# Kernel tuning notes

Hardware: AMD Instinct MI355X
Metric: run time of the kernel (lower is better)

Reference implementation:

```python
import jax, jax.numpy as jnp
import numpy as np

# Module hyperparameters (from init_kwargs)
C = 128        # in_channel
L = 16         # seq_len
K = 7          # filter_size
DIL = 1        # dilation
G = 4          # num_groups
SPAN = (K - 1) * DIL + 1
PAD = (SPAN - 1) // 2

B, H, W = 8, 56, 56


def setup_inputs() -> dict:
    key = jax.random.key(0)
    k1, k2 = jax.random.split(key)
    x = jax.random.normal(k1, (B, C, L, H, W), dtype=jnp.float32)
    # kaiming_normal(mode='fan_out', nonlinearity='relu'):
    # fan_out = shape[0] * K * K, std = sqrt(2 / fan_out)
    std = (2.0 / (C * K * K)) ** 0.5
    filter_weight = jax.random.normal(k2, (C, L, K, K), dtype=jnp.float32) * std
    return {"x": x, "filter_weight": filter_weight}


def reference(x, filter_weight):
    # x: (B, C, T, H, W) ; filter_weight: (C, T, K, K)
    b, c, t, h, w = x.shape
    # zero-pad spatial dims
    x2 = jnp.pad(x, ((0, 0), (0, 0), (0, 0), (PAD, PAD), (PAD, PAD)))
    # x1: temporally shifted input (frame t-1, first frame duplicated)
    x1 = jnp.concatenate([x[:, :, :1], x[:, :, :-1]], axis=2)

    outs = []
    # static K*K offset loop (dy slow, dx fast -> matches torch meshgrid 'ij' flatten order)
    for dy in range(0, SPAN, DIL):
        for dx in range(0, SPAN, DIL):
            w_ct = filter_weight[:, :, dy // DIL, dx // DIL]  # (C, T)
            shifted = jax.lax.slice(
                x2, (0, 0, 0, dy, dx), (b, c, t, dy + h, dx + w))
            prod = w_ct[None, :, :, None, None] * x1 * shifted  # (B,C,T,H,W)
            # groupwise channel mean -> (B, G, T, H, W)
            resp = prod.reshape(b, G, c // G, t, h, w).mean(axis=2)
            outs.append(resp)
    # concat over offsets along channel dim -> (B, K^2*G, T, H, W)
    return jnp.concatenate(outs, axis=1)
```

## Files before the change

kernel.cpp:

```cpp
#include <hip/hip_runtime.h>
#include <cstdint>

#define C_ 128
#define L_ 16
#define G_ 4
#define H_ 56
#define W_ 56
#define HW_ 3136
#define CH_ 4
#define NCK_ 8
#define RS_ 64
#define XS_F (CH_ * 14 * RS_)
#define LDS_F (2 * XS_F)
#define PAD_F 6656

typedef float f4 __attribute__((ext_vector_type(4)));
typedef __attribute__((address_space(3))) uint32_t lds_u32;
typedef const __attribute__((address_space(1))) uint32_t glb_u32;

__global__ __launch_bounds__(448, 2)
void wcorr(const float* __restrict__ x, const float* __restrict__ wgt,
           float* __restrict__ out) {
  __shared__ float lds[LDS_F];
  __shared__ float lds_pad[PAD_F];
  asm volatile("" :: "v"(&lds_pad[threadIdx.x & 63]));

  int bid = blockIdx.x;
  int wid = (bid & 7) * 448 + (bid >> 3);
  int htile = wid % 7;
  int rest = wid / 7;
  int t = rest & 15;
  int bg = rest >> 4;
  int g = bg & 3;
  int b = bg >> 2;
  int h0 = htile * 8;

  int tid = threadIdx.x;
  int lane = tid & 63;
  int dyu = __builtin_amdgcn_readfirstlane(tid >> 6);
  int tx = lane & 7;
  int h = lane >> 3;
  bool wr = (tx < 7);
  int txc = wr ? tx : 6;
  int w0 = 8 * txc;
  int r = h + dyu;
  int t1 = (t > 0) ? (t - 1) : 0;

  for (int i = tid; i < LDS_F; i += 448) lds[i] = 0.0f;

  const size_t cstride = (size_t)L_ * HW_;
  const float* xg = x + ((size_t)b * C_ + (size_t)g * 32) * cstride;
  const float* x1b = xg + (size_t)t1 * HW_ + (size_t)(h0 + h) * W_ + w0;
  const float* wgb = wgt + (size_t)(g * 32) * (L_ * 49) + t * 49 + dyu * 7;

  auto stage = [&](int tau, int k) {
    int fb = (k & 1) * XS_F;
    int c0 = k * CH_;
    int rho = tau >> 4;
    int sb = tau & 15;
    int ci = rho / 14;
    int rr = rho - ci * 14;
    int vb = sb ^ (rr & 7);
    int hh = h0 - 3 + rr;
    bool ok = (vb >= 1) && (vb <= 14) && (hh >= 0) && (hh < H_);
    const float* src = xg + (size_t)(c0 + ci) * cstride + (size_t)t * HW_
                          + hh * W_ + (vb * 4 - 4);
    float* dst = &lds[fb + (tau & ~63) * 4];
    if (ok)
      __builtin_amdgcn_global_load_lds((glb_u32*)src, (lds_u32*)dst, 16, 0, 0);
  };

  float acc[7][8];
  #pragma unroll
  for (int i = 0; i < 7; ++i)
    #pragma unroll
    for (int p = 0; p < 8; ++p) acc[i][p] = 0.0f;

  __syncthreads();
  stage(tid, 0);
  stage(tid + 448, 0);
  __syncthreads();

  #pragma unroll 2
  for (int k = 0; k < NCK_; ++k) {
    if (k + 1 < NCK_) {
      stage(tid, k + 1);
      stage(tid + 448, k + 1);
    }
    int fb = (k & 1) * XS_F;
    int c0 = k * CH_;
    int s = r & 7;
    #pragma unroll
    for (int ci = 0; ci < CH_; ++ci) {
      const f4* xsrow = (const f4*)&lds[fb + (ci * 14 + r) * RS_];
      f4 q0 = xsrow[(2 * txc + 0) ^ s];
      f4 q1 = xsrow[(2 * txc + 1) ^ s];
      f4 q2 = xsrow[(2 * txc + 2) ^ s];
      f4 q3 = xsrow[(2 * txc + 3) ^ s];
      const float* x1p = x1b + (size_t)(c0 + ci) * cstride;
      f4 a0 = *(const f4*)(x1p);
      f4 a1 = *(const f4*)(x1p + 4);
      const float* wp = wgb + (size_t)(c0 + ci) * (L_ * 49);
      float w7[7];
      #pragma unroll
      for (int d = 0; d < 7; ++d) w7[d] = wp[d];
      float rr_[16] = {q0.x, q0.y, q0.z, q0.w, q1.x, q1.y, q1.z, q1.w,
                       q2.x, q2.y, q2.z, q2.w, q3.x, q3.y, q3.z, q3.w};
      float x1v[8] = {a0.x, a0.y, a0.z, a0.w, a1.x, a1.y, a1.z, a1.w};
      #pragma unroll
      for (int dxx = 0; dxx < 7; ++dxx) {
        #pragma unroll
        for (int p = 0; p < 8; ++p) {
          acc[dxx][p] = fmaf(w7[dxx], x1v[p] * rr_[p + dxx + 1], acc[dxx][p]);
        }
      }
    }
    __syncthreads();
  }

  if (wr) {
    const float sc = 1.0f / 32.0f;
    #pragma unroll
    for (int dxx = 0; dxx < 7; ++dxx) {
      int och = (dyu * 7 + dxx) * G_ + g;
      float* op = out + (((size_t)b * 196 + och) * L_ + t) * (size_t)HW_
                      + (size_t)(h0 + h) * W_ + w0;
      f4 o0 = {acc[dxx][0] * sc, acc[dxx][1] * sc,
               acc[dxx][2] * sc, acc[dxx][3] * sc};
      f4 o1 = {acc[dxx][4] * sc, acc[dxx][5] * sc,
               acc[dxx][6] * sc, acc[dxx][7] * sc};
      __builtin_nontemporal_store(o0, (f4*)op);
      __builtin_nontemporal_store(o1, (f4*)(op + 4));
    }
  }
}

extern "C" void kernel_launch(void* const* d_in, const int* in_sizes, int n_in,
                              void* d_out, int out_size, void* d_ws, size_t ws_size,
                              hipStream_t stream) {
  const float* x = (const float*)d_in[0];
  const float* w = (const float*)d_in[1];
  float* o = (float*)d_out;
  dim3 grid(3584), block(448);
  hipLaunchKernelGGL(wcorr, grid, block, 0, stream, x, w, o);
}
```

Measured before the change: 244.6 us.

## Halve row tile, stage filter weights in LDS, and remap threads to 256-wide blocks

Each block now covers 4 output rows instead of 8 and uses 256 threads, with each wave holding several dy/h slots, so the grid doubles to 7168 blocks. The per-(c,dy) filter weights are prescaled by 1/32 and preloaded into LDS once per block, replacing per-thread global weight loads. The x tile is padded to a 68-float row stride in place of the XOR swizzle. Idle lanes rise (dy==7 slots and tx==7 lanes), the halo rows are reloaded more often relative to output, and the unswizzled layout may cause LDS bank conflicts.

```diff
diff --git a/kernel.cpp b/kernel.cpp
--- a/kernel.cpp
+++ b/kernel.cpp
@@ -9,16 +9,19 @@
 #define HW_ 3136
 #define CH_ 4
 #define NCK_ 8
-#define RS_ 64
-#define XS_F (CH_ * 14 * RS_)
-#define LDS_F (2 * XS_F)
-#define PAD_F 6656
+#define RS_ 68
+#define NROW_ 10
+#define XS_F (CH_ * NROW_ * RS_)
+#define XTASK_ (CH_ * NROW_ * 17)
+#define WL_F 2048
+#define LDS_F (WL_F + 2 * XS_F)
+#define PAD_F 768
 
 typedef float f4 __attribute__((ext_vector_type(4)));
 typedef __attribute__((address_space(3))) uint32_t lds_u32;
 typedef const __attribute__((address_space(1))) uint32_t glb_u32;
 
-__global__ __launch_bounds__(448, 2)
+__global__ __launch_bounds__(256, 2)
 void wcorr(const float* __restrict__ x, const float* __restrict__ wgt,
            float* __restrict__ out) {
   __shared__ float lds[LDS_F];
@@ -26,48 +29,69 @@
   asm volatile("" :: "v"(&lds_pad[threadIdx.x & 63]));
 
   int bid = blockIdx.x;
-  int wid = (bid & 7) * 448 + (bid >> 3);
-  int htile = wid % 7;
-  int rest = wid / 7;
+  int wid = (bid & 7) * 896 + (bid >> 3);
+  int htile = wid % 14;
+  int rest = wid / 14;
   int t = rest & 15;
   int bg = rest >> 4;
   int g = bg & 3;
   int b = bg >> 2;
-  int h0 = htile * 8;
+  int h0 = htile * 4;
 
   int tid = threadIdx.x;
-  int lane = tid & 63;
-  int dyu = __builtin_amdgcn_readfirstlane(tid >> 6);
-  int tx = lane & 7;
-  int h = lane >> 3;
-  bool wr = (tx < 7);
-  int txc = wr ? tx : 6;
+  int tx = tid & 7;
+  int slot = tid >> 3;
+  int h = slot & 3;
+  int dy = slot >> 2;
+  bool active = (dy < 7) && (tx < 7);
+  int dyc = dy < 7 ? dy : 6;
+  int txc = tx < 7 ? tx : 6;
+  int r = h + dyc;
+  int t1 = t > 0 ? t - 1 : 0;
   int w0 = 8 * txc;
-  int r = h + dyu;
-  int t1 = (t > 0) ? (t - 1) : 0;
 
-  for (int i = tid; i < LDS_F; i += 448) lds[i] = 0.0f;
+  for (int i = tid; i < LDS_F; i += 256) lds[i] = 0.0f;
+  __syncthreads();
 
   const size_t cstride = (size_t)L_ * HW_;
   const float* xg = x + ((size_t)b * C_ + (size_t)g * 32) * cstride;
   const float* x1b = xg + (size_t)t1 * HW_ + (size_t)(h0 + h) * W_ + w0;
-  const float* wgb = wgt + (size_t)(g * 32) * (L_ * 49) + t * 49 + dyu * 7;
 
-  auto stage = [&](int tau, int k) {
-    int fb = (k & 1) * XS_F;
+  {
+    const float sc = 1.0f / 32.0f;
+    const float* wsrc = wgt + (size_t)(g * 32) * (L_ * 49) + t * 49;
+    #pragma unroll
+    for (int j = 0; j < 8; ++j) {
+      int idx = tid + j * 256;
+      int c = idx >> 6;
+      int rem = idx & 63;
+      int dyy = rem >> 3, dxx = rem & 7;
+      float v = 0.0f;
+      if (dyy < 7 && dxx < 7)
+        v = wsrc[(size_t)c * (L_ * 49) + dyy * 7 + dxx] * sc;
+      lds[idx] = v;
+    }
+  }
+
+  auto stage = [&](int tau, int k, bool on) {
+    int fb = WL_F + (k & 1) * XS_F;
     int c0 = k * CH_;
-    int rho = tau >> 4;
-    int sb = tau & 15;
-    int ci = rho / 14;
-    int rr = rho - ci * 14;
-    int vb = sb ^ (rr & 7);
+    int row = (tau * 965) >> 14;
+    int vb = tau - row * 17;
+    int ci = (row * 205) >> 11;
+    int rr = row - ci * 10;
     int hh = h0 - 3 + rr;
-    bool ok = (vb >= 1) && (vb <= 14) && (hh >= 0) && (hh < H_);
+    bool ok = on && (vb >= 1) && (vb <= 14) && (hh >= 0) && (hh < H_);
     const float* src = xg + (size_t)(c0 + ci) * cstride + (size_t)t * HW_
                           + hh * W_ + (vb * 4 - 4);
     float* dst = &lds[fb + (tau & ~63) * 4];
     if (ok)
       __builtin_amdgcn_global_load_lds((glb_u32*)src, (lds_u32*)dst, 16, 0, 0);
+  };
+  auto stage_chunk = [&](int k) {
+    stage(tid, k, true);
+    stage(tid + 256, k, true);
+    stage(tid + 512, k, tid + 512 < XTASK_);
   };
 
   float acc[7][8];
@@ -76,34 +100,28 @@
     #pragma unroll
     for (int p = 0; p < 8; ++p) acc[i][p] = 0.0f;
 
-  __syncthreads();
-  stage(tid, 0);
-  stage(tid + 448, 0);
+  stage_chunk(0);
   __syncthreads();
 
   #pragma unroll 2
   for (int k = 0; k < NCK_; ++k) {
-    if (k + 1 < NCK_) {
-      stage(tid, k + 1);
-      stage(tid + 448, k + 1);
-    }
-    int fb = (k & 1) * XS_F;
+    if (k + 1 < NCK_) stage_chunk(k + 1);
+    int fb = WL_F + (k & 1) * XS_F;
     int c0 = k * CH_;
-    int s = r & 7;
     #pragma unroll
     for (int ci = 0; ci < CH_; ++ci) {
-      const f4* xsrow = (const f4*)&lds[fb + (ci * 14 + r) * RS_];
-      f4 q0 = xsrow[(2 * txc + 0) ^ s];
-      f4 q1 = xsrow[(2 * txc + 1) ^ s];
-      f4 q2 = xsrow[(2 * txc + 2) ^ s];
-      f4 q3 = xsrow[(2 * txc + 3) ^ s];
+      const f4* xsrow = (const f4*)&lds[fb + (ci * NROW_ + r) * RS_];
+      f4 q0 = xsrow[2 * txc + 0];
+      f4 q1 = xsrow[2 * txc + 1];
+      f4 q2 = xsrow[2 * txc + 2];
+      f4 q3 = xsrow[2 * txc + 3];
+      const f4* wl = (const f4*)&lds[(c0 + ci) * 64 + dyc * 8];
+      f4 wv0 = wl[0];
+      f4 wv1 = wl[1];
       const float* x1p = x1b + (size_t)(c0 + ci) * cstride;
       f4 a0 = *(const f4*)(x1p);
       f4 a1 = *(const f4*)(x1p + 4);
-      const float* wp = wgb + (size_t)(c0 + ci) * (L_ * 49);
-      float w7[7];
-      #pragma unroll
-      for (int d = 0; d < 7; ++d) w7[d] = wp[d];
+      float w7[7] = {wv0.x, wv0.y, wv0.z, wv0.w, wv1.x, wv1.y, wv1.z};
       float rr_[16] = {q0.x, q0.y, q0.z, q0.w, q1.x, q1.y, q1.z, q1.w,
                        q2.x, q2.y, q2.z, q2.w, q3.x, q3.y, q3.z, q3.w};
       float x1v[8] = {a0.x, a0.y, a0.z, a0.w, a1.x, a1.y, a1.z, a1.w};
@@ -118,17 +136,14 @@
     __syncthreads();
   }
 
-  if (wr) {
-    const float sc = 1.0f / 32.0f;
+  if (active) {
     #pragma unroll
     for (int dxx = 0; dxx < 7; ++dxx) {
-      int och = (dyu * 7 + dxx) * G_ + g;
+      int och = (dy * 7 + dxx) * G_ + g;
       float* op = out + (((size_t)b * 196 + och) * L_ + t) * (size_t)HW_
                       + (size_t)(h0 + h) * W_ + w0;
-      f4 o0 = {acc[dxx][0] * sc, acc[dxx][1] * sc,
-               acc[dxx][2] * sc, acc[dxx][3] * sc};
-      f4 o1 = {acc[dxx][4] * sc, acc[dxx][5] * sc,
-               acc[dxx][6] * sc, acc[dxx][7] * sc};
+      f4 o0 = {acc[dxx][0], acc[dxx][1], acc[dxx][2], acc[dxx][3]};
+      f4 o1 = {acc[dxx][4], acc[dxx][5], acc[dxx][6], acc[dxx][7]};
       __builtin_nontemporal_store(o0, (f4*)op);
       __builtin_nontemporal_store(o1, (f4*)(op + 4));
     }
@@ -141,6 +156,6 @@
   const float* x = (const float*)d_in[0];
   const float* w = (const float*)d_in[1];
   float* o = (float*)d_out;
-  dim3 grid(3584), block(448);
+  dim3 grid(7168), block(256);
   hipLaunchKernelGGL(wcorr, grid, block, 0, stream, x, w, o);
 }
```

New measurement: 249.7 us. +2.1%, slower.
